# Kernel tuning notes

Hardware: AMD Instinct MI355X
Metric: run time of the kernel (lower is better)

Reference implementation:

```python
import jax, jax.numpy as jnp
import numpy as np

NUM_GROUPS = 32
EPS = 1e-6


def group_norm(x, gamma, beta):
    # x: [B, C, H, W]; GroupNorm over (channels-in-group, H, W)
    B, C, H, W = x.shape
    xg = x.reshape(B, NUM_GROUPS, C // NUM_GROUPS, H, W)
    mean = xg.mean(axis=(2, 3, 4), keepdims=True)
    var = xg.var(axis=(2, 3, 4), keepdims=True)
    xn = ((xg - mean) * jax.lax.rsqrt(var + EPS)).reshape(B, C, H, W)
    return xn * gamma[None, :, None, None] + beta[None, :, None, None]


def conv1x1(x, w, b):
    # 1x1 conv == channel-mixing matmul. w: [C_out, C_in]
    return jnp.einsum('bchw,oc->bohw', x, w) + b[None, :, None, None]


def setup_inputs() -> dict:
    key = jax.random.key(0)
    ks = jax.random.split(key, 6)
    B, C, H, W = 8, 256, 64, 64
    s = 1.0 / np.sqrt(C)  # fan-in scaled weights (like Conv2d default)
    inp = {
        'x': jax.random.normal(ks[0], (B, C, H, W), jnp.float32),
        'gamma': jnp.ones((C,), jnp.float32),
        'beta': jnp.zeros((C,), jnp.float32),
        'wq': jax.random.normal(ks[1], (C, C), jnp.float32) * s,
        'bq': jnp.zeros((C,), jnp.float32),
        'wk': jax.random.normal(ks[2], (C, C), jnp.float32) * s,
        'bk': jnp.zeros((C,), jnp.float32),
        'wv': jax.random.normal(ks[3], (C, C), jnp.float32) * s,
        'bv': jnp.zeros((C,), jnp.float32),
        'wo': jax.random.normal(ks[4], (C, C), jnp.float32) * s,
        'bo': jnp.zeros((C,), jnp.float32),
    }
    return inp


def reference(x, gamma, beta, wq, bq, wk, bk, wv, bv, wo, bo):
    B, C, H, W = x.shape
    h = group_norm(x, gamma, beta)
    q = conv1x1(h, wq, bq)
    k = conv1x1(h, wk, bk)
    v = conv1x1(h, wv, bv)
    # elu + 1 feature map (nonnegative kernel features)
    q = jax.nn.elu(q) + 1.0
    k = jax.nn.elu(k) + 1.0
    N = H * W
    kf = k.reshape(B, C, N)            # [B, C, N]
    vf = v.reshape(B, C, N)            # [B, C, N]
    qf = q.reshape(B, C, N)            # [B, C, N]
    # kv = k @ v^T : [B, C, C]
    kv = jnp.einsum('bcn,bdn->bcd', kf, vf)
    # h_out[b, n, d] = sum_c q[b, c, n] * kv[b, c, d]; stored channel-first
    h_out = jnp.einsum('bcn,bcd->bdn', qf, kv).reshape(B, C, H, W)
    return x + conv1x1(h_out, wo, bo)
```

## Files before the change

### kernel.cpp

```cpp
#include <hip/hip_runtime.h>
#include <math.h>

#define C_DIM 256
#define N_DIM 4096
#define B_DIM 8

typedef __attribute__((ext_vector_type(8))) short bf16x8;
typedef __attribute__((ext_vector_type(4))) float f32x4;
typedef __attribute__((ext_vector_type(8))) unsigned short us8;
typedef __attribute__((ext_vector_type(4))) unsigned short us4;

__device__ inline unsigned short f2bf(float f) {
    unsigned int u = __float_as_uint(f);
    u += 0x7fffu + ((u >> 16) & 1u);
    return (unsigned short)(u >> 16);
}

__device__ inline void gload_lds16(const void* g, void* l) {
    __builtin_amdgcn_global_load_lds(
        (const __attribute__((address_space(1))) unsigned int*)g,
        (__attribute__((address_space(3))) unsigned int*)l, 16, 0, 0);
}

__global__ __launch_bounds__(256) void prep_kernel(
    const float* __restrict__ wq, const float* __restrict__ wk,
    const float* __restrict__ wv, const float* __restrict__ wo,
    const float* __restrict__ bk, const float* __restrict__ bv,
    const float* __restrict__ x,
    unsigned short* __restrict__ wqb, unsigned short* __restrict__ wkvb,
    unsigned short* __restrict__ wob, float* __restrict__ bkv,
    float2* __restrict__ sums)
{
    int z = blockIdx.x;
    int t = threadIdx.x;
    if (z < 256) {
        const float* s; unsigned short* d;
        int which = z >> 6;
        if (which == 0)      { s = wq; d = wqb; }
        else if (which == 1) { s = wk; d = wkvb; }
        else if (which == 2) { s = wv; d = wkvb + 65536; }
        else                 { s = wo; d = wob; }
        int idx = (z & 63) * 1024 + t * 4;
        float4 v = *(const float4*)(s + idx);
        us4 r; r[0] = f2bf(v.x); r[1] = f2bf(v.y); r[2] = f2bf(v.z); r[3] = f2bf(v.w);
        *(us4*)(d + idx) = r;
    } else if (z == 256) {
        bkv[t]       = bk[t];
        bkv[t + 256] = bv[t];
    } else {
        int bc = z - 257;
        const float* xc = x + (size_t)bc * N_DIM;
        float s = 0.f, q = 0.f;
        for (int i = t; i < 1024; i += 256) {
            float4 v = ((const float4*)xc)[i];
            s += v.x + v.y + v.z + v.w;
            q += v.x*v.x + v.y*v.y + v.z*v.z + v.w*v.w;
        }
        #pragma unroll
        for (int off = 32; off > 0; off >>= 1) {
            s += __shfl_down(s, off);
            q += __shfl_down(q, off);
        }
        __shared__ float red[8];
        int w = t >> 6;
        if ((t & 63) == 0) { red[w*2] = s; red[w*2+1] = q; }
        __syncthreads();
        if (t == 0) {
            sums[bc] = make_float2(red[0]+red[2]+red[4]+red[6],
                                   red[1]+red[3]+red[5]+red[7]);
        }
    }
}

__global__ __launch_bounds__(256) void gn_apply(const float* __restrict__ x,
                                                const float2* __restrict__ sums,
                                                const float* __restrict__ gamma,
                                                const float* __restrict__ beta,
                                                unsigned short* __restrict__ hT) {
    int b = blockIdx.y, n0 = blockIdx.x * 64;
    int t = threadIdx.x;
    __shared__ float scale[256], shift[256];
    __shared__ unsigned short trans[64][264];

    {
        int c = t;
        int gbase = c & ~7;
        float s = 0.f, q = 0.f;
        #pragma unroll
        for (int j = 0; j < 8; j++) {
            float2 u = sums[b*256 + gbase + j];
            s += u.x; q += u.y;
        }
        float mean = s * (1.f/32768.f);
        float var  = q * (1.f/32768.f) - mean*mean;
        float inv  = rsqrtf(var + 1e-6f);
        float gm = gamma[c] * inv;
        scale[c] = gm;
        shift[c] = beta[c] - mean * gm;
    }
    __syncthreads();

    #pragma unroll
    for (int it = 0; it < 16; it++) {
        int c  = it*16 + (t >> 4);
        int nl = (t & 15) * 4;
        float4 v = *(const float4*)(x + ((size_t)(b*C_DIM + c))*N_DIM + n0 + nl);
        float sc = scale[c], sh = shift[c];
        trans[nl+0][c] = f2bf(v.x*sc + sh);
        trans[nl+1][c] = f2bf(v.y*sc + sh);
        trans[nl+2][c] = f2bf(v.z*sc + sh);
        trans[nl+3][c] = f2bf(v.w*sc + sh);
    }
    __syncthreads();

    #pragma unroll
    for (int it = 0; it < 8; it++) {
        int nl = it*8 + (t >> 5);
        int cb = (t & 31) * 8;
        us8 vv = *(us8*)&trans[nl][cb];
        *(us8*)(hT + ((size_t)b*N_DIM + n0 + nl)*C_DIM + cb) = vv;
    }
}

__global__ __launch_bounds__(256) void kvred(const float* __restrict__ src, unsigned short* __restrict__ dst) {
    int gi = (blockIdx.x * 256 + threadIdx.x) * 4;
    int b = gi >> 16, idx = gi & 65535;
    float4 a = make_float4(0.f,0.f,0.f,0.f);
    #pragma unroll
    for (int sp = 0; sp < 16; sp++) {
        float4 v = *(const float4*)(src + (((size_t)b*16 + sp) << 16) + idx);
        a.x += v.x; a.y += v.y; a.z += v.z; a.w += v.w;
    }
    us4 r; r[0] = f2bf(a.x); r[1] = f2bf(a.y); r[2] = f2bf(a.z); r[3] = f2bf(a.w);
    *(us4*)(dst + ((size_t)b << 16) + idx) = r;
}

template<int MODE>
__device__ __forceinline__ void gemm_body(
    const unsigned short* __restrict__ Ab, const unsigned short* __restrict__ Bb,
    const float* __restrict__ bias, const float* __restrict__ residb,
    void* __restrict__ Cb,
    int N, int K, int k0, int Ks, int m_blk, int n_blk, bool elu,
    char* smem)
{
    unsigned short* As = (unsigned short*)smem;
    unsigned short* Bs = As + 4096;

    int t = threadIdx.x;
    int w = t >> 6, l = t & 63;
    int wm = w >> 1, wn = w & 1;
    int l15 = l & 15, quad = l >> 4;

    int srow = w * 16 + (l >> 2);
    int skc  = (l & 3) * 8;

    f32x4 acc[4][4];
    #pragma unroll
    for (int i = 0; i < 4; i++)
        #pragma unroll
        for (int j = 0; j < 4; j++)
            #pragma unroll
            for (int r = 0; r < 4; r++) acc[i][j][r] = 0.f;

    const unsigned short* Asw = As + (wm*64 + l15)*32 + quad*8;
    const unsigned short* Bsw = Bs + (wn*64 + l15)*32 + quad*8;
    unsigned short* Asl = As + w*512 + l*8;
    unsigned short* Bsl = Bs + w*512 + l*8;

    for (int kt = k0; kt < k0 + Ks; kt += 32) {
        #pragma unroll
        for (int rep = 0; rep < 2; rep++) {
            gload_lds16(Ab + (size_t)(m_blk + rep*64 + srow) * K + kt + skc, Asl + rep*2048);
            gload_lds16(Bb + (size_t)(n_blk + rep*64 + srow) * K + kt + skc, Bsl + rep*2048);
        }
        __syncthreads();
        bf16x8 af[4], bfr[4];
        #pragma unroll
        for (int i = 0; i < 4; i++) af[i]  = *(const bf16x8*)(Asw + i*16*32);
        #pragma unroll
        for (int j = 0; j < 4; j++) bfr[j] = *(const bf16x8*)(Bsw + j*16*32);
        #pragma unroll
        for (int i = 0; i < 4; i++)
            #pragma unroll
            for (int j = 0; j < 4; j++)
                acc[i][j] = __builtin_amdgcn_mfma_f32_16x16x32_bf16(af[i], bfr[j], acc[i][j], 0, 0, 0);
        __syncthreads();
    }

    if (MODE == 0 || MODE == 1 || MODE == 4) {
        unsigned short* ep = (unsigned short*)smem;
        int row0 = wm*64 + quad*4;
        int col0 = wn*64 + l15;
        #pragma unroll
        for (int i = 0; i < 4; i++) {
            #pragma unroll
            for (int j = 0; j < 4; j++) {
                int cl = col0 + j*16;
                #pragma unroll
                for (int r = 0; r < 4; r++) {
                    int rl = row0 + i*16 + r;
                    float val = acc[i][j][r];
                    if (MODE == 0) {
                        val += bias[n_blk + cl];
                        val = val > 0.f ? val + 1.f : __expf(val);
                    } else if (MODE == 1) {
                        val += bias[m_blk + rl];
                        if (elu) val = val > 0.f ? val + 1.f : __expf(val);
                    }
                    ep[rl*136 + cl] = f2bf(val);
                }
            }
        }
        __syncthreads();
        unsigned short* Cp = (unsigned short*)Cb;
        #pragma unroll
        for (int it = 0; it < 8; it++) {
            int row = it*16 + (t >> 4);
            int col = (t & 15) * 8;
            us8 vv = *(us8*)(ep + row*136 + col);
            *(us8*)(Cp + (size_t)(m_blk + row) * N + n_blk + col) = vv;
        }
    } else {
        float* ep32 = (float*)smem;
        float* Cp = (float*)Cb;
        #pragma unroll
        for (int h = 0; h < 2; h++) {
            if (wm == h) {
                int row0 = quad*4;
                int col0 = wn*64 + l15;
                #pragma unroll
                for (int i = 0; i < 4; i++)
                    #pragma unroll
                    for (int j = 0; j < 4; j++)
                        #pragma unroll
                        for (int r = 0; r < 4; r++)
                            ep32[(row0 + i*16 + r)*140 + col0 + j*16] = acc[i][j][r];
            }
            __syncthreads();
            #pragma unroll
            for (int it = 0; it < 8; it++) {
                int rl  = it*8 + (t >> 5);
                int row = m_blk + h*64 + rl;
                int col = (t & 31) * 4;
                f32x4 vv = *(f32x4*)(ep32 + rl*140 + col);
                if (MODE == 5) {
                    float bi = bias[row];
                    float4 rv = *(const float4*)(residb + (size_t)row * N + n_blk + col);
                    vv[0] += bi + rv.x; vv[1] += bi + rv.y;
                    vv[2] += bi + rv.z; vv[3] += bi + rv.w;
                }
                *(f32x4*)(Cp + (size_t)row * N + n_blk + col) = vv;
            }
            __syncthreads();
        }
    }
}

__global__ __launch_bounds__(256) void qkv_kernel(
    const unsigned short* __restrict__ hT, const unsigned short* __restrict__ wqb,
    const unsigned short* __restrict__ wkvb,
    const float* __restrict__ bq, const float* __restrict__ bkv,
    unsigned short* __restrict__ qT, unsigned short* __restrict__ kvbuf)
{
    __shared__ __align__(16) char smem[36864];
    int z = blockIdx.x;
    if (z < 512) {
        int b = z >> 6, rem = z & 63;
        int m_blk = (rem >> 1) * 128, n_blk = (rem & 1) * 128;
        gemm_body<0>(hT + (size_t)b*1048576, wqb, bq, nullptr,
                     qT + (size_t)b*1048576,
                     256, 256, 0, 256, m_blk, n_blk, true, smem);
    } else {
        int iz = z - 512;
        int b = iz >> 7, rem = iz & 127;
        int m_blk = (rem >> 5) * 128, n_blk = (rem & 31) * 128;
        gemm_body<1>(wkvb, hT + (size_t)b*1048576, bkv, nullptr,
                     kvbuf + (size_t)b*2097152,
                     4096, 256, 0, 256, m_blk, n_blk, m_blk < 256, smem);
    }
}

template<int MODE>
__global__ __launch_bounds__(256) void gemm_nt(
    const unsigned short* __restrict__ A, const unsigned short* __restrict__ B,
    const float* __restrict__ bias, const float* __restrict__ resid,
    void* __restrict__ Cout,
    int N, int K, int splits,
    size_t sA, size_t sB, size_t sC, size_t sR, int elem4)
{
    __shared__ __align__(16) char smem[36864];
    int b  = blockIdx.z / splits;
    int sp = blockIdx.z % splits;
    int Ks = K / splits;
    size_t cbase = (MODE == 3) ? ((size_t)(b*splits + sp)) * sC : (size_t)b * sC;
    void* Cb = elem4 ? (void*)((float*)Cout + cbase) : (void*)((unsigned short*)Cout + cbase);
    gemm_body<MODE>(A + b*sA, B + b*sB, bias,
                    resid ? resid + b*sR : nullptr, Cb,
                    N, K, sp*Ks, Ks, blockIdx.y*128, blockIdx.x*128, false, smem);
}

extern "C" void kernel_launch(void* const* d_in, const int* in_sizes, int n_in,
                              void* d_out, int out_size, void* d_ws, size_t ws_size,
                              hipStream_t stream) {
    const float* x     = (const float*)d_in[0];
    const float* gamma = (const float*)d_in[1];
    const float* beta  = (const float*)d_in[2];
    const float* wq    = (const float*)d_in[3];
    const float* bq    = (const float*)d_in[4];
    const float* wk    = (const float*)d_in[5];
    const float* bk    = (const float*)d_in[6];
    const float* wv    = (const float*)d_in[7];
    const float* bv    = (const float*)d_in[8];
    const float* wo    = (const float*)d_in[9];
    const float* bo    = (const float*)d_in[10];
    float* out = (float*)d_out;

    const size_t TEN = (size_t)B_DIM * C_DIM * N_DIM;
    unsigned short* ws16  = (unsigned short*)d_ws;
    unsigned short* hT    = ws16;
    unsigned short* qT    = hT    + TEN;
    unsigned short* kvbuf = qT    + TEN;
    unsigned short* kvb   = kvbuf + 2*TEN;
    unsigned short* M2b   = kvb   + 524288;
    unsigned short* wqb   = M2b   + 524288;
    unsigned short* wkvb  = wqb   + 65536;
    unsigned short* wob   = wkvb  + 131072;
    float*          bkv   = (float*)(wob + 65536);
    float2*         sums  = (float2*)(bkv + 512);
    float*          kvf   = (float*)(sums + 2048);

    prep_kernel<<<dim3(2305), 256, 0, stream>>>(wq, wk, wv, wo, bk, bv, x,
                                                wqb, wkvb, wob, bkv, sums);
    gn_apply<<<dim3(N_DIM/64, B_DIM), 256, 0, stream>>>(x, sums, gamma, beta, hT);
    qkv_kernel<<<dim3(1536), 256, 0, stream>>>(hT, wqb, wkvb, bq, bkv, qT, kvbuf);
    gemm_nt<3><<<dim3(2, 2, B_DIM*16), 256, 0, stream>>>(
        kvbuf, kvbuf + 1048576, nullptr, nullptr, kvf,
        256, 4096, 16, 2097152, 2097152, 65536, 0, 1);
    kvred<<<dim3(512), 256, 0, stream>>>(kvf, kvb);
    gemm_nt<4><<<dim3(2, 2, B_DIM), 256, 0, stream>>>(
        wob, kvb, nullptr, nullptr, M2b,
        256, 256, 1, 0, 65536, 65536, 0, 0);
    gemm_nt<5><<<dim3(32, 2, B_DIM), 256, 0, stream>>>(
        M2b, qT, bo, x, out,
        4096, 256, 1, 65536, 1048576, 1048576, 1048576, 1);
}
```

Before: 185.5 us.

## Fold GroupNorm into QKV weights, fuse kv reduction with Wo GEMM, unroll K loop

```diff
diff --git a/kernel.cpp b/kernel.cpp
--- a/kernel.cpp
+++ b/kernel.cpp
@@ -22,94 +22,31 @@
         (__attribute__((address_space(3))) unsigned int*)l, 16, 0, 0);
 }
 
-__global__ __launch_bounds__(256) void prep_kernel(
-    const float* __restrict__ wq, const float* __restrict__ wk,
-    const float* __restrict__ wv, const float* __restrict__ wo,
-    const float* __restrict__ bk, const float* __restrict__ bv,
-    const float* __restrict__ x,
-    unsigned short* __restrict__ wqb, unsigned short* __restrict__ wkvb,
-    unsigned short* __restrict__ wob, float* __restrict__ bkv,
-    float2* __restrict__ sums)
-{
-    int z = blockIdx.x;
+__global__ __launch_bounds__(256) void transx(const float* __restrict__ x,
+                                              unsigned short* __restrict__ xT,
+                                              float2* __restrict__ pst) {
+    int b = blockIdx.y, nt = blockIdx.x, n0 = nt * 64;
     int t = threadIdx.x;
-    if (z < 256) {
-        const float* s; unsigned short* d;
-        int which = z >> 6;
-        if (which == 0)      { s = wq; d = wqb; }
-        else if (which == 1) { s = wk; d = wkvb; }
-        else if (which == 2) { s = wv; d = wkvb + 65536; }
-        else                 { s = wo; d = wob; }
-        int idx = (z & 63) * 1024 + t * 4;
-        float4 v = *(const float4*)(s + idx);
-        us4 r; r[0] = f2bf(v.x); r[1] = f2bf(v.y); r[2] = f2bf(v.z); r[3] = f2bf(v.w);
-        *(us4*)(d + idx) = r;
-    } else if (z == 256) {
-        bkv[t]       = bk[t];
-        bkv[t + 256] = bv[t];
-    } else {
-        int bc = z - 257;
-        const float* xc = x + (size_t)bc * N_DIM;
-        float s = 0.f, q = 0.f;
-        for (int i = t; i < 1024; i += 256) {
-            float4 v = ((const float4*)xc)[i];
-            s += v.x + v.y + v.z + v.w;
-            q += v.x*v.x + v.y*v.y + v.z*v.z + v.w*v.w;
-        }
-        #pragma unroll
-        for (int off = 32; off > 0; off >>= 1) {
-            s += __shfl_down(s, off);
-            q += __shfl_down(q, off);
-        }
-        __shared__ float red[8];
-        int w = t >> 6;
-        if ((t & 63) == 0) { red[w*2] = s; red[w*2+1] = q; }
-        __syncthreads();
-        if (t == 0) {
-            sums[bc] = make_float2(red[0]+red[2]+red[4]+red[6],
-                                   red[1]+red[3]+red[5]+red[7]);
-        }
-    }
-}
-
-__global__ __launch_bounds__(256) void gn_apply(const float* __restrict__ x,
-                                                const float2* __restrict__ sums,
-                                                const float* __restrict__ gamma,
-                                                const float* __restrict__ beta,
-                                                unsigned short* __restrict__ hT) {
-    int b = blockIdx.y, n0 = blockIdx.x * 64;
-    int t = threadIdx.x;
-    __shared__ float scale[256], shift[256];
     __shared__ unsigned short trans[64][264];
-
-    {
-        int c = t;
-        int gbase = c & ~7;
-        float s = 0.f, q = 0.f;
-        #pragma unroll
-        for (int j = 0; j < 8; j++) {
-            float2 u = sums[b*256 + gbase + j];
-            s += u.x; q += u.y;
-        }
-        float mean = s * (1.f/32768.f);
-        float var  = q * (1.f/32768.f) - mean*mean;
-        float inv  = rsqrtf(var + 1e-6f);
-        float gm = gamma[c] * inv;
-        scale[c] = gm;
-        shift[c] = beta[c] - mean * gm;
-    }
-    __syncthreads();
 
     #pragma unroll
     for (int it = 0; it < 16; it++) {
         int c  = it*16 + (t >> 4);
         int nl = (t & 15) * 4;
         float4 v = *(const float4*)(x + ((size_t)(b*C_DIM + c))*N_DIM + n0 + nl);
-        float sc = scale[c], sh = shift[c];
-        trans[nl+0][c] = f2bf(v.x*sc + sh);
-        trans[nl+1][c] = f2bf(v.y*sc + sh);
-        trans[nl+2][c] = f2bf(v.z*sc + sh);
-        trans[nl+3][c] = f2bf(v.w*sc + sh);
+        trans[nl+0][c] = f2bf(v.x);
+        trans[nl+1][c] = f2bf(v.y);
+        trans[nl+2][c] = f2bf(v.z);
+        trans[nl+3][c] = f2bf(v.w);
+        float s4 = v.x + v.y + v.z + v.w;
+        float q4 = v.x*v.x + v.y*v.y + v.z*v.z + v.w*v.w;
+        #pragma unroll
+        for (int m = 1; m < 16; m <<= 1) {
+            s4 += __shfl_xor(s4, m);
+            q4 += __shfl_xor(q4, m);
+        }
+        if ((t & 15) == 0)
+            pst[(size_t)(b*64 + nt)*256 + c] = make_float2(s4, q4);
     }
     __syncthreads();
 
@@ -118,21 +55,89 @@
         int nl = it*8 + (t >> 5);
         int cb = (t & 31) * 8;
         us8 vv = *(us8*)&trans[nl][cb];
-        *(us8*)(hT + ((size_t)b*N_DIM + n0 + nl)*C_DIM + cb) = vv;
-    }
-}
-
-__global__ __launch_bounds__(256) void kvred(const float* __restrict__ src, unsigned short* __restrict__ dst) {
-    int gi = (blockIdx.x * 256 + threadIdx.x) * 4;
-    int b = gi >> 16, idx = gi & 65535;
-    float4 a = make_float4(0.f,0.f,0.f,0.f);
-    #pragma unroll
-    for (int sp = 0; sp < 16; sp++) {
-        float4 v = *(const float4*)(src + (((size_t)b*16 + sp) << 16) + idx);
-        a.x += v.x; a.y += v.y; a.z += v.z; a.w += v.w;
-    }
-    us4 r; r[0] = f2bf(a.x); r[1] = f2bf(a.y); r[2] = f2bf(a.z); r[3] = f2bf(a.w);
-    *(us4*)(dst + ((size_t)b << 16) + idx) = r;
+        *(us8*)(xT + ((size_t)b*N_DIM + n0 + nl)*C_DIM + cb) = vv;
+    }
+}
+
+__global__ __launch_bounds__(256) void fold(
+    const float* __restrict__ wq, const float* __restrict__ wk,
+    const float* __restrict__ wv, const float* __restrict__ wo,
+    const float* __restrict__ bq, const float* __restrict__ bk,
+    const float* __restrict__ bv,
+    const float* __restrict__ gamma, const float* __restrict__ beta,
+    const float2* __restrict__ pst,
+    unsigned short* __restrict__ wqb2, unsigned short* __restrict__ wkvb2,
+    unsigned short* __restrict__ wob,
+    float* __restrict__ bq2, float* __restrict__ bkv2)
+{
+    int z = blockIdx.y;
+    int t = threadIdx.x;
+    if (z == 12) {
+        int base = blockIdx.x * 8192;
+        #pragma unroll
+        for (int i = 0; i < 8; i++) {
+            int idx = base + i*1024 + t*4;
+            float4 v = *(const float4*)(wo + idx);
+            us4 r; r[0]=f2bf(v.x); r[1]=f2bf(v.y); r[2]=f2bf(v.z); r[3]=f2bf(v.w);
+            *(us4*)(wob + idx) = r;
+        }
+        return;
+    }
+    int b = blockIdx.x;
+    __shared__ float scale[256], shift[256], chS[256], chQ[256];
+
+    float S = 0.f, Q = 0.f;
+    for (int nt = 0; nt < 64; nt++) {
+        float2 u = pst[(size_t)(b*64 + nt)*256 + t];
+        S += u.x; Q += u.y;
+    }
+    chS[t] = S; chQ[t] = Q;
+    __syncthreads();
+    {
+        int gb = t & ~7;
+        float Sg = 0.f, Qg = 0.f;
+        #pragma unroll
+        for (int j = 0; j < 8; j++) { Sg += chS[gb+j]; Qg += chQ[gb+j]; }
+        float mean = Sg * (1.f/32768.f);
+        float var  = Qg * (1.f/32768.f) - mean*mean;
+        float inv  = rsqrtf(var + 1e-6f);
+        float sc = gamma[t] * inv;
+        scale[t] = sc;
+        shift[t] = beta[t] - mean * sc;
+    }
+    __syncthreads();
+
+    int r0 = z * 64;
+    const float* Wsrc; const float* bsrc; unsigned short* dst; float* bdst;
+    if (r0 < 256)      { int r=r0;     Wsrc=wq+(size_t)r*256; bsrc=bq+r; dst=wqb2 +(size_t)b*65536 +(size_t)r*256;      bdst=bq2 +b*256+r; }
+    else if (r0 < 512) { int r=r0-256; Wsrc=wk+(size_t)r*256; bsrc=bk+r; dst=wkvb2+(size_t)b*131072+(size_t)r*256;      bdst=bkv2+b*512+r; }
+    else               { int r=r0-512; Wsrc=wv+(size_t)r*256; bsrc=bv+r; dst=wkvb2+(size_t)b*131072+(size_t)(r+256)*256; bdst=bkv2+b*512+256+r; }
+
+    #pragma unroll
+    for (int i = 0; i < 16; i++) {
+        int idx = t + 256*i;
+        int row = idx >> 6, c4 = (idx & 63) * 4;
+        float4 v = *(const float4*)(Wsrc + (size_t)row*256 + c4);
+        us4 r;
+        r[0] = f2bf(v.x * scale[c4+0]);
+        r[1] = f2bf(v.y * scale[c4+1]);
+        r[2] = f2bf(v.z * scale[c4+2]);
+        r[3] = f2bf(v.w * scale[c4+3]);
+        *(us4*)(dst + (size_t)row*256 + c4) = r;
+    }
+
+    {
+        int row = t >> 2, qd = t & 3;
+        float p = 0.f;
+        for (int i = 0; i < 64; i++) {
+            int c = qd*64 + i;
+            p += Wsrc[(size_t)row*256 + c] * shift[c];
+        }
+        chS[t] = p;
+        __syncthreads();
+        if (t < 64)
+            bdst[t] = bsrc[t] + chS[t*4] + chS[t*4+1] + chS[t*4+2] + chS[t*4+3];
+    }
 }
 
 template<int MODE>
@@ -143,8 +148,10 @@
     int N, int K, int k0, int Ks, int m_blk, int n_blk, bool elu,
     char* smem)
 {
-    unsigned short* As = (unsigned short*)smem;
-    unsigned short* Bs = As + 4096;
+    unsigned short* As0 = (unsigned short*)smem;
+    unsigned short* Bs0 = As0 + 4096;
+    unsigned short* As1 = As0 + 8192;
+    unsigned short* Bs1 = As0 + 12288;
 
     int t = threadIdx.x;
     int w = t >> 6, l = t & 63;
@@ -162,32 +169,46 @@
             #pragma unroll
             for (int r = 0; r < 4; r++) acc[i][j][r] = 0.f;
 
-    const unsigned short* Asw = As + (wm*64 + l15)*32 + quad*8;
-    const unsigned short* Bsw = Bs + (wn*64 + l15)*32 + quad*8;
-    unsigned short* Asl = As + w*512 + l*8;
-    unsigned short* Bsl = Bs + w*512 + l*8;
-
-    for (int kt = k0; kt < k0 + Ks; kt += 32) {
+    int fro = (wm*64 + l15)*32 + quad*8;
+    int fco = (wn*64 + l15)*32 + quad*8;
+    int sl  = w*512 + l*8;
+
+    for (int kt = k0; kt < k0 + Ks; kt += 64) {
         #pragma unroll
         for (int rep = 0; rep < 2; rep++) {
-            gload_lds16(Ab + (size_t)(m_blk + rep*64 + srow) * K + kt + skc, Asl + rep*2048);
-            gload_lds16(Bb + (size_t)(n_blk + rep*64 + srow) * K + kt + skc, Bsl + rep*2048);
+            size_t ga = (size_t)(m_blk + rep*64 + srow) * K + kt + skc;
+            size_t gb = (size_t)(n_blk + rep*64 + srow) * K + kt + skc;
+            gload_lds16(Ab + ga,      As0 + sl + rep*2048);
+            gload_lds16(Bb + gb,      Bs0 + sl + rep*2048);
+            gload_lds16(Ab + ga + 32, As1 + sl + rep*2048);
+            gload_lds16(Bb + gb + 32, Bs1 + sl + rep*2048);
         }
         __syncthreads();
-        bf16x8 af[4], bfr[4];
-        #pragma unroll
-        for (int i = 0; i < 4; i++) af[i]  = *(const bf16x8*)(Asw + i*16*32);
-        #pragma unroll
-        for (int j = 0; j < 4; j++) bfr[j] = *(const bf16x8*)(Bsw + j*16*32);
-        #pragma unroll
-        for (int i = 0; i < 4; i++)
-            #pragma unroll
-            for (int j = 0; j < 4; j++)
-                acc[i][j] = __builtin_amdgcn_mfma_f32_16x16x32_bf16(af[i], bfr[j], acc[i][j], 0, 0, 0);
+        {
+            bf16x8 af[4], bfr[4];
+            #pragma unroll
+            for (int i = 0; i < 4; i++) af[i]  = *(const bf16x8*)(As0 + fro + i*512);
+            #pragma unroll
+            for (int j = 0; j < 4; j++) bfr[j] = *(const bf16x8*)(Bs0 + fco + j*512);
+            #pragma unroll
+            for (int i = 0; i < 4; i++)
+                #pragma unroll
+                for (int j = 0; j < 4; j++)
+                    acc[i][j] = __builtin_amdgcn_mfma_f32_16x16x32_bf16(af[i], bfr[j], acc[i][j], 0, 0, 0);
+            #pragma unroll
+            for (int i = 0; i < 4; i++) af[i]  = *(const bf16x8*)(As1 + fro + i*512);
+            #pragma unroll
+            for (int j = 0; j < 4; j++) bfr[j] = *(const bf16x8*)(Bs1 + fco + j*512);
+            #pragma unroll
+            for (int i = 0; i < 4; i++)
+                #pragma unroll
+                for (int j = 0; j < 4; j++)
+                    acc[i][j] = __builtin_amdgcn_mfma_f32_16x16x32_bf16(af[i], bfr[j], acc[i][j], 0, 0, 0);
+        }
         __syncthreads();
     }
 
-    if (MODE == 0 || MODE == 1 || MODE == 4) {
+    if (MODE == 0 || MODE == 1) {
         unsigned short* ep = (unsigned short*)smem;
         int row0 = wm*64 + quad*4;
         int col0 = wn*64 + l15;
@@ -203,7 +224,7 @@
                     if (MODE == 0) {
                         val += bias[n_blk + cl];
                         val = val > 0.f ? val + 1.f : __expf(val);
-                    } else if (MODE == 1) {
+                    } else {
                         val += bias[m_blk + rl];
                         if (elu) val = val > 0.f ? val + 1.f : __expf(val);
                     }
@@ -257,9 +278,9 @@
 }
 
 __global__ __launch_bounds__(256) void qkv_kernel(
-    const unsigned short* __restrict__ hT, const unsigned short* __restrict__ wqb,
-    const unsigned short* __restrict__ wkvb,
-    const float* __restrict__ bq, const float* __restrict__ bkv,
+    const unsigned short* __restrict__ xT,
+    const unsigned short* __restrict__ wqb2, const unsigned short* __restrict__ wkvb2,
+    const float* __restrict__ bq2, const float* __restrict__ bkv2,
     unsigned short* __restrict__ qT, unsigned short* __restrict__ kvbuf)
 {
     __shared__ __align__(16) char smem[36864];
@@ -267,36 +288,126 @@
     if (z < 512) {
         int b = z >> 6, rem = z & 63;
         int m_blk = (rem >> 1) * 128, n_blk = (rem & 1) * 128;
-        gemm_body<0>(hT + (size_t)b*1048576, wqb, bq, nullptr,
+        gemm_body<0>(xT + (size_t)b*1048576, wqb2 + (size_t)b*65536,
+                     bq2 + b*256, nullptr,
                      qT + (size_t)b*1048576,
                      256, 256, 0, 256, m_blk, n_blk, true, smem);
     } else {
         int iz = z - 512;
         int b = iz >> 7, rem = iz & 127;
         int m_blk = (rem >> 5) * 128, n_blk = (rem & 31) * 128;
-        gemm_body<1>(wkvb, hT + (size_t)b*1048576, bkv, nullptr,
+        gemm_body<1>(wkvb2 + (size_t)b*131072, xT + (size_t)b*1048576,
+                     bkv2 + b*512, nullptr,
                      kvbuf + (size_t)b*2097152,
                      4096, 256, 0, 256, m_blk, n_blk, m_blk < 256, smem);
     }
 }
 
-template<int MODE>
-__global__ __launch_bounds__(256) void gemm_nt(
-    const unsigned short* __restrict__ A, const unsigned short* __restrict__ B,
-    const float* __restrict__ bias, const float* __restrict__ resid,
-    void* __restrict__ Cout,
-    int N, int K, int splits,
-    size_t sA, size_t sB, size_t sC, size_t sR, int elem4)
+__global__ __launch_bounds__(256) void kv_kernel(const unsigned short* __restrict__ kvbuf,
+                                                 float* __restrict__ kvf)
 {
     __shared__ __align__(16) char smem[36864];
-    int b  = blockIdx.z / splits;
-    int sp = blockIdx.z % splits;
-    int Ks = K / splits;
-    size_t cbase = (MODE == 3) ? ((size_t)(b*splits + sp)) * sC : (size_t)b * sC;
-    void* Cb = elem4 ? (void*)((float*)Cout + cbase) : (void*)((unsigned short*)Cout + cbase);
-    gemm_body<MODE>(A + b*sA, B + b*sB, bias,
-                    resid ? resid + b*sR : nullptr, Cb,
-                    N, K, sp*Ks, Ks, blockIdx.y*128, blockIdx.x*128, false, smem);
+    int b = blockIdx.z >> 4, sp = blockIdx.z & 15;
+    gemm_body<3>(kvbuf + (size_t)b*2097152, kvbuf + (size_t)b*2097152 + 1048576,
+                 nullptr, nullptr,
+                 kvf + (size_t)(b*16 + sp)*65536,
+                 256, 4096, sp*256, 256, blockIdx.y*128, blockIdx.x*128, false, smem);
+}
+
+__global__ __launch_bounds__(256) void m2red(const float* __restrict__ kvf,
+                                             const unsigned short* __restrict__ wob,
+                                             unsigned short* __restrict__ M2b)
+{
+    __shared__ __align__(16) unsigned short smem2[67584];
+    unsigned short* Bsf = smem2;
+    unsigned short* Asf = smem2 + 33792;
+
+    int b = blockIdx.z, m_blk = blockIdx.y*128, n_blk = blockIdx.x*128;
+    int t = threadIdx.x;
+
+    #pragma unroll
+    for (int i = 0; i < 32; i++) {
+        int j = t + 256*i;
+        int c = j >> 6, c4 = (j & 63) * 4;
+        float4 a = make_float4(0.f,0.f,0.f,0.f);
+        #pragma unroll
+        for (int sp = 0; sp < 16; sp++) {
+            float4 v = *(const float4*)(kvf + ((size_t)(b*16+sp) << 16) + (size_t)(n_blk + c)*256 + c4);
+            a.x += v.x; a.y += v.y; a.z += v.z; a.w += v.w;
+        }
+        us4 r; r[0]=f2bf(a.x); r[1]=f2bf(a.y); r[2]=f2bf(a.z); r[3]=f2bf(a.w);
+        *(us4*)(Bsf + c*264 + c4) = r;
+    }
+    #pragma unroll
+    for (int i = 0; i < 16; i++) {
+        int j = t + 256*i;
+        int row = j >> 5, col8 = (j & 31) * 8;
+        us8 v = *(const us8*)(wob + (size_t)(m_blk + row)*256 + col8);
+        *(us8*)(Asf + row*264 + col8) = v;
+    }
+    __syncthreads();
+
+    int w = t >> 6, l = t & 63;
+    int wm = w >> 1, wn = w & 1;
+    int l15 = l & 15, quad = l >> 4;
+
+    f32x4 acc[4][4];
+    #pragma unroll
+    for (int i = 0; i < 4; i++)
+        #pragma unroll
+        for (int j = 0; j < 4; j++)
+            #pragma unroll
+            for (int r = 0; r < 4; r++) acc[i][j][r] = 0.f;
+
+    #pragma unroll
+    for (int kc = 0; kc < 8; kc++) {
+        bf16x8 af[4], bfr[4];
+        #pragma unroll
+        for (int i = 0; i < 4; i++)
+            af[i]  = *(const bf16x8*)(Asf + (wm*64 + i*16 + l15)*264 + kc*32 + quad*8);
+        #pragma unroll
+        for (int j = 0; j < 4; j++)
+            bfr[j] = *(const bf16x8*)(Bsf + (wn*64 + j*16 + l15)*264 + kc*32 + quad*8);
+        #pragma unroll
+        for (int i = 0; i < 4; i++)
+            #pragma unroll
+            for (int j = 0; j < 4; j++)
+                acc[i][j] = __builtin_amdgcn_mfma_f32_16x16x32_bf16(af[i], bfr[j], acc[i][j], 0, 0, 0);
+    }
+    __syncthreads();
+
+    unsigned short* ep = Asf;
+    int row0 = wm*64 + quad*4;
+    int col0 = wn*64 + l15;
+    #pragma unroll
+    for (int i = 0; i < 4; i++)
+        #pragma unroll
+        for (int j = 0; j < 4; j++)
+            #pragma unroll
+            for (int r = 0; r < 4; r++)
+                ep[(row0 + i*16 + r)*136 + col0 + j*16] = f2bf(acc[i][j][r]);
+    __syncthreads();
+    #pragma unroll
+    for (int it = 0; it < 8; it++) {
+        int row = it*16 + (t >> 4);
+        int col = (t & 15) * 8;
+        us8 vv = *(us8*)(ep + row*136 + col);
+        *(us8*)(M2b + (size_t)b*65536 + (size_t)(m_blk + row)*256 + n_blk + col) = vv;
+    }
+}
+
+__global__ __launch_bounds__(256) void out_kernel(const unsigned short* __restrict__ M2b,
+                                                  const unsigned short* __restrict__ qT,
+                                                  const float* __restrict__ bo,
+                                                  const float* __restrict__ x,
+                                                  float* __restrict__ outp)
+{
+    __shared__ __align__(16) char smem[36864];
+    int b = blockIdx.z;
+    gemm_body<5>(M2b + (size_t)b*65536, qT + (size_t)b*1048576,
+                 bo, x + (size_t)b*1048576,
+                 outp + (size_t)b*1048576,
+                 4096, 256, 0, 256, blockIdx.y*128, blockIdx.x*128, false, smem);
 }
 
 extern "C" void kernel_launch(void* const* d_in, const int* in_sizes, int n_in,
@@ -317,30 +428,23 @@
 
     const size_t TEN = (size_t)B_DIM * C_DIM * N_DIM;
     unsigned short* ws16  = (unsigned short*)d_ws;
-    unsigned short* hT    = ws16;
-    unsigned short* qT    = hT    + TEN;
+    unsigned short* xT    = ws16;
+    unsigned short* qT    = xT    + TEN;
     unsigned short* kvbuf = qT    + TEN;
-    unsigned short* kvb   = kvbuf + 2*TEN;
-    unsigned short* M2b   = kvb   + 524288;
-    unsigned short* wqb   = M2b   + 524288;
-    unsigned short* wkvb  = wqb   + 65536;
-    unsigned short* wob   = wkvb  + 131072;
-    float*          bkv   = (float*)(wob + 65536);
-    float2*         sums  = (float2*)(bkv + 512);
-    float*          kvf   = (float*)(sums + 2048);
-
-    prep_kernel<<<dim3(2305), 256, 0, stream>>>(wq, wk, wv, wo, bk, bv, x,
-                                                wqb, wkvb, wob, bkv, sums);
-    gn_apply<<<dim3(N_DIM/64, B_DIM), 256, 0, stream>>>(x, sums, gamma, beta, hT);
-    qkv_kernel<<<dim3(1536), 256, 0, stream>>>(hT, wqb, wkvb, bq, bkv, qT, kvbuf);
-    gemm_nt<3><<<dim3(2, 2, B_DIM*16), 256, 0, stream>>>(
-        kvbuf, kvbuf + 1048576, nullptr, nullptr, kvf,
-        256, 4096, 16, 2097152, 2097152, 65536, 0, 1);
-    kvred<<<dim3(512), 256, 0, stream>>>(kvf, kvb);
-    gemm_nt<4><<<dim3(2, 2, B_DIM), 256, 0, stream>>>(
-        wob, kvb, nullptr, nullptr, M2b,
-        256, 256, 1, 0, 65536, 65536, 0, 0);
-    gemm_nt<5><<<dim3(32, 2, B_DIM), 256, 0, stream>>>(
-        M2b, qT, bo, x, out,
-        4096, 256, 1, 65536, 1048576, 1048576, 1048576, 1);
-}
+    unsigned short* wqb2  = kvbuf + 2*TEN;
+    unsigned short* wkvb2 = wqb2  + 524288;
+    unsigned short* wob   = wkvb2 + 1048576;
+    unsigned short* M2b   = wob   + 65536;
+    float*          bq2   = (float*)(M2b + 524288);
+    float*          bkv2  = bq2   + 2048;
+    float2*         pst   = (float2*)(bkv2 + 4096);
+    float*          kvf   = (float*)(pst + 131072);
+
+    transx<<<dim3(64, B_DIM), 256, 0, stream>>>(x, xT, pst);
+    fold<<<dim3(8, 13), 256, 0, stream>>>(wq, wk, wv, wo, bq, bk, bv, gamma, beta,
+                                          pst, wqb2, wkvb2, wob, bq2, bkv2);
+    qkv_kernel<<<dim3(1536), 256, 0, stream>>>(xT, wqb2, wkvb2, bq2, bkv2, qT, kvbuf);
+    kv_kernel<<<dim3(2, 2, B_DIM*16), 256, 0, stream>>>(kvbuf, kvf);
+    m2red<<<dim3(2, 2, B_DIM), 256, 0, stream>>>(kvf, wob, M2b);
+    out_kernel<<<dim3(32, 2, B_DIM), 256, 0, stream>>>(M2b, qT, bo, x, out);
+}
```

Result: slower. 213.4 us (+15.0%).
